# Performance work log

Measured on AMD Instinct MI355X. Metric: run time of the kernel, lower is better.

Reference implementation:

```python
import jax, jax.numpy as jnp
import numpy as np

DIM = 128
N_NODES = 50000
N_EDGES = 625000


def setup_inputs() -> dict:
    key = jax.random.key(0)
    ks = jax.random.split(key, 6)
    X = jax.random.normal(ks[0], (N_NODES, DIM), dtype=jnp.float32)
    edge_index = jax.random.randint(ks[1], (2, N_EDGES), 0, N_NODES, dtype=jnp.int64)
    # Linear params, init like torch (uniform +/- 1/sqrt(dim))
    bound = 1.0 / np.sqrt(DIM)
    msg_w = jax.random.uniform(ks[2], (DIM, DIM), minval=-bound, maxval=bound, dtype=jnp.float32)
    msg_b = jax.random.uniform(ks[3], (DIM,), minval=-bound, maxval=bound, dtype=jnp.float32)
    lin_w = jax.random.uniform(ks[4], (DIM, DIM), minval=-bound, maxval=bound, dtype=jnp.float32)
    lin_b = jax.random.uniform(ks[5], (DIM,), minval=-bound, maxval=bound, dtype=jnp.float32)
    eps = jnp.asarray(0.0, dtype=jnp.float32)
    return {"X": X, "edge_index": edge_index, "eps": eps,
            "msg_w": msg_w, "msg_b": msg_b, "lin_w": lin_w, "lin_b": lin_b}


def reference(X, edge_index, eps, msg_w, msg_b, lin_w, lin_b):
    src, dst = edge_index[0], edge_index[1]
    # msg_lin(X) then gather at dst: (E, F)
    msg = (jnp.einsum('nf,gf->ng', X, msg_w) + msg_b)[dst]
    # scatter-add messages onto src nodes: (N, F)
    agg = jax.ops.segment_sum(msg, src, num_segments=X.shape[0])
    out = (1.0 + eps) * X + agg
    out = jnp.einsum('nf,gf->ng', out, lin_w) + lin_b
    return jax.nn.relu(out)
```

## Files before the change

kernel.cpp:

```cpp
#include <hip/hip_runtime.h>
#include <hip/hip_bf16.h>

#define NN 50000
#define NE 625000
#define DIM 128

#define NBKT 782
#define NBKTP 784
#define CAP 1536
#define CHUNK 2048
#define NCHUNK ((NE + CHUNK - 1) / CHUNK)

#define XCAST_NB 6250
#define PREP_NB 65
#define BIN_B0 (XCAST_NB + PREP_NB)
#define SETUP_NB (BIN_B0 + NCHUNK)

using fragAB = __attribute__((ext_vector_type(8))) short;
using fragC  = __attribute__((ext_vector_type(4))) float;

__device__ __forceinline__ unsigned short f2bf(float f) {
    unsigned int u = __float_as_uint(f);
    unsigned int r = u + 0x7FFFu + ((u >> 16) & 1u);
    return (unsigned short)(r >> 16);
}

__device__ __forceinline__ float bflo(unsigned v) { return __uint_as_float(v << 16); }
__device__ __forceinline__ float bfhi(unsigned v) { return __uint_as_float(v & 0xffff0000u); }

__global__ __launch_bounds__(256) void setup_kernel(
    const float* __restrict__ X, const int* __restrict__ ei,
    const float* __restrict__ L, const float* __restrict__ W,
    const float* __restrict__ mb, float* __restrict__ cb,
    unsigned short* __restrict__ Bh, unsigned short* __restrict__ Xbf,
    int* __restrict__ bucket_cursor, unsigned* __restrict__ staging) {
    int blk = blockIdx.x;
    int t = threadIdx.x;

    if (blk < XCAST_NB) {
        int idx = (blk * 256 + t) * 4;
        float4 v = *(const float4*)(X + idx);
        uint2 p;
        p.x = (unsigned)f2bf(v.x) | ((unsigned)f2bf(v.y) << 16);
        p.y = (unsigned)f2bf(v.z) | ((unsigned)f2bf(v.w) << 16);
        *(uint2*)(Xbf + idx) = p;
        return;
    }
    if (blk < BIN_B0) {
        int idx = (blk - XCAST_NB) * 256 + t;
        if (idx < DIM * DIM) {
            int o = idx >> 7, g = idx & 127;
            float s = 0.f;
            for (int f = 0; f < DIM; f++) s += L[o * DIM + f] * W[f * DIM + g];
            Bh[o * 256 + 128 + g] = f2bf(s);
            Bh[o * 256 + g] = f2bf(L[o * DIM + g]);
        } else if (idx < DIM * DIM + DIM) {
            int o = idx - DIM * DIM;
            float s = 0.f;
            for (int f = 0; f < DIM; f++) s += L[o * DIM + f] * mb[f];
            cb[o] = s;
        }
        return;
    }

    __shared__ int cnt[NBKTP];
    __shared__ int base[NBKTP];
    __shared__ int gb[NBKTP];
    __shared__ int sarr[256];
    __shared__ unsigned staged[CHUNK];
    int e0 = (blk - BIN_B0) * CHUNK;
    int nthis = NE - e0; if (nthis > CHUNK) nthis = CHUNK;

    for (int i = t; i < NBKTP; i += 256) cnt[i] = 0;
    __syncthreads();

    unsigned pk[CHUNK / 256];
#pragma unroll
    for (int i = 0; i < CHUNK / 256; i++) {
        int e = e0 + i * 256 + t;
        if (e < NE) {
            int s = ei[e];
            int d = ei[NE + e];
            unsigned b = (unsigned)s >> 6;
            pk[i] = (b << 22) | ((unsigned)(s & 63) << 16) | (unsigned)d;
            atomicAdd(&cnt[b], 1);
        } else pk[i] = 0xFFFFFFFFu;
    }
    __syncthreads();

    int myb = t * 4;
    int s0 = 0;
    if (myb < NBKTP) s0 = cnt[myb] + cnt[myb + 1] + cnt[myb + 2] + cnt[myb + 3];
    sarr[t] = s0;
    __syncthreads();
    for (int off = 1; off < 256; off <<= 1) {
        int v = (t >= off) ? sarr[t - off] : 0;
        __syncthreads();
        sarr[t] += v;
        __syncthreads();
    }
    int run = sarr[t] - s0;
    if (myb < NBKTP) {
        for (int i = 0; i < 4; i++) {
            int b = myb + i;
            base[b] = run;
            int c = cnt[b];
            gb[b] = (b < NBKT && c > 0) ? atomicAdd(&bucket_cursor[b], c) : 0;
            run += c;
        }
    }
    __syncthreads();
    if (myb < NBKTP) {
        for (int i = 0; i < 4; i++) cnt[myb + i] = base[myb + i];
    }
    __syncthreads();

#pragma unroll
    for (int i = 0; i < CHUNK / 256; i++) {
        if (pk[i] != 0xFFFFFFFFu) {
            unsigned b = pk[i] >> 22;
            int pos = atomicAdd(&cnt[b], 1);
            staged[pos] = pk[i];
        }
    }
    __syncthreads();

    for (int idx = t; idx < nthis; idx += 256) {
        unsigned p = staged[idx];
        unsigned b = p >> 22;
        int pos = gb[b] + (idx - base[b]);
        if (pos < CAP) staging[(size_t)b * CAP + pos] = p;
    }
}

__global__ __launch_bounds__(256) void bucket_sort(const int* __restrict__ bucket_cursor,
                                                   const unsigned* __restrict__ staging,
                                                   int* __restrict__ deg, int* __restrict__ offs,
                                                   int* __restrict__ sdst) {
    __shared__ unsigned rec[CAP];
    __shared__ unsigned sorted_[CAP];
    __shared__ int hcnt[64];
    __shared__ int hbase[64];
    __shared__ int cur[64];
    int t = threadIdx.x;
    int b = blockIdx.x;
    int cnt_b = bucket_cursor[b];
    if (cnt_b > CAP) cnt_b = CAP;
    int base_b = b * CAP;

    if (t < 64) hcnt[t] = 0;
    __syncthreads();
    for (int i = t; i < cnt_b; i += 256) {
        unsigned r = staging[(size_t)b * CAP + i];
        rec[i] = r;
        atomicAdd(&hcnt[(r >> 16) & 63], 1);
    }
    __syncthreads();
    if (t == 0) {
        int run = 0;
        for (int i = 0; i < 64; i++) { hbase[i] = run; run += hcnt[i]; }
    }
    __syncthreads();
    if (t < 64) {
        cur[t] = hbase[t];
        int src = b * 64 + t;
        if (src < NN) {
            deg[src] = hcnt[t];
            offs[src] = base_b + hbase[t];
        }
    }
    __syncthreads();
    for (int i = t; i < cnt_b; i += 256) {
        unsigned r = rec[i];
        int pos = atomicAdd(&cur[(r >> 16) & 63], 1);
        sorted_[pos] = r;
    }
    __syncthreads();
    for (int i = t; i < cnt_b; i += 256)
        sdst[base_b + i] = (int)(sorted_[i] & 0xFFFFu);
}

__global__ __launch_bounds__(256) void gather_kernel(const int* __restrict__ offs,
                                                     const int* __restrict__ deg,
                                                     const int* __restrict__ sdst,
                                                     const unsigned short* __restrict__ Xbf,
                                                     unsigned short* __restrict__ Aggbf) {
    int wave = (blockIdx.x * 256 + threadIdx.x) >> 6;
    int lane = threadIdx.x & 63;
    if (wave >= NN) return;
    int start = __builtin_amdgcn_readfirstlane(offs[wave]);
    int cnt = __builtin_amdgcn_readfirstlane(deg[wave]);
    const unsigned* __restrict__ Xd = (const unsigned*)Xbf;
    float ax = 0.f, ay = 0.f;
    int j = 0;
    for (; j + 8 <= cnt; j += 8) {
        int d0 = sdst[start + j + 0];
        int d1 = sdst[start + j + 1];
        int d2 = sdst[start + j + 2];
        int d3 = sdst[start + j + 3];
        int d4 = sdst[start + j + 4];
        int d5 = sdst[start + j + 5];
        int d6 = sdst[start + j + 6];
        int d7 = sdst[start + j + 7];
        unsigned v0 = Xd[(size_t)d0 * 64 + lane];
        unsigned v1 = Xd[(size_t)d1 * 64 + lane];
        unsigned v2 = Xd[(size_t)d2 * 64 + lane];
        unsigned v3 = Xd[(size_t)d3 * 64 + lane];
        unsigned v4 = Xd[(size_t)d4 * 64 + lane];
        unsigned v5 = Xd[(size_t)d5 * 64 + lane];
        unsigned v6 = Xd[(size_t)d6 * 64 + lane];
        unsigned v7 = Xd[(size_t)d7 * 64 + lane];
        ax += bflo(v0) + bflo(v1) + bflo(v2) + bflo(v3) +
              bflo(v4) + bflo(v5) + bflo(v6) + bflo(v7);
        ay += bfhi(v0) + bfhi(v1) + bfhi(v2) + bfhi(v3) +
              bfhi(v4) + bfhi(v5) + bfhi(v6) + bfhi(v7);
    }
    if (j + 4 <= cnt) {
        int d0 = sdst[start + j + 0];
        int d1 = sdst[start + j + 1];
        int d2 = sdst[start + j + 2];
        int d3 = sdst[start + j + 3];
        unsigned v0 = Xd[(size_t)d0 * 64 + lane];
        unsigned v1 = Xd[(size_t)d1 * 64 + lane];
        unsigned v2 = Xd[(size_t)d2 * 64 + lane];
        unsigned v3 = Xd[(size_t)d3 * 64 + lane];
        ax += bflo(v0) + bflo(v1) + bflo(v2) + bflo(v3);
        ay += bfhi(v0) + bfhi(v1) + bfhi(v2) + bfhi(v3);
        j += 4;
    }
    for (; j < cnt; j++) {
        int d = sdst[start + j];
        unsigned v = Xd[(size_t)d * 64 + lane];
        ax += bflo(v);
        ay += bfhi(v);
    }
    unsigned packed = (unsigned)f2bf(ax) | ((unsigned)f2bf(ay) << 16);
    ((unsigned*)Aggbf)[(size_t)wave * 64 + lane] = packed;
}

__global__ __launch_bounds__(256) void outgemm_kernel(
    const unsigned short* __restrict__ Xbf, const unsigned short* __restrict__ Aggbf,
    const unsigned short* __restrict__ Bh, const int* __restrict__ deg,
    const float* __restrict__ cb, const float* __restrict__ lin_b,
    const float* __restrict__ epsp, float* __restrict__ out) {
    __shared__ unsigned short As[128 * 40];
    __shared__ unsigned short Bs[128 * 40];
    int tid = threadIdx.x;
    int lane = tid & 63;
    int wave = tid >> 6;
    int m16 = lane & 15;
    int quad = lane >> 4;
    int waveM = (wave & 1) * 64;
    int waveN = (wave >> 1) * 64;
    int r0 = blockIdx.x * 128;
    float scale = 1.0f + *epsp;

    fragC acc[4][4];
#pragma unroll
    for (int i = 0; i < 4; i++)
#pragma unroll
        for (int j = 0; j < 4; j++) acc[i][j] = (fragC){0.f, 0.f, 0.f, 0.f};

    int srow = tid >> 1;
    int shalf = tid & 1;
    int arow = r0 + srow;
    if (arow >= NN) arow = NN - 1;

    for (int kc = 0; kc < 8; kc++) {
        int kb = kc * 32;
        {
            const unsigned short* asrc = (kc < 4) ? Xbf : Aggbf;
            int akb = kb & 127;
            const uint4* gp = (const uint4*)(asrc + (size_t)arow * 128 + akb + shalf * 16);
            uint4 w0 = gp[0];
            uint4 w1 = gp[1];
            uint4* lp = (uint4*)(As + srow * 40 + shalf * 16);
            lp[0] = w0;
            lp[1] = w1;
        }
        {
            const uint4* gp = (const uint4*)(Bh + (size_t)srow * 256 + kb + shalf * 16);
            uint4 w0 = gp[0];
            uint4 w1 = gp[1];
            if (kb < 128) {
                unsigned int* u0 = (unsigned int*)&w0;
                unsigned int* u1 = (unsigned int*)&w1;
#pragma unroll
                for (int q = 0; q < 4; q++) {
                    float lo = bflo(u0[q]) * scale;
                    float hi = bfhi(u0[q]) * scale;
                    u0[q] = (unsigned)f2bf(lo) | ((unsigned)f2bf(hi) << 16);
                    lo = bflo(u1[q]) * scale;
                    hi = bfhi(u1[q]) * scale;
                    u1[q] = (unsigned)f2bf(lo) | ((unsigned)f2bf(hi) << 16);
                }
            }
            uint4* lp = (uint4*)(Bs + srow * 40 + shalf * 16);
            lp[0] = w0;
            lp[1] = w1;
        }
        __syncthreads();

        fragAB a[4], bfr[4];
#pragma unroll
        for (int i = 0; i < 4; i++)
            a[i] = *(const fragAB*)(As + (waveM + i * 16 + m16) * 40 + quad * 8);
#pragma unroll
        for (int j = 0; j < 4; j++)
            bfr[j] = *(const fragAB*)(Bs + (waveN + j * 16 + m16) * 40 + quad * 8);
#pragma unroll
        for (int i = 0; i < 4; i++)
#pragma unroll
            for (int j = 0; j < 4; j++)
                acc[i][j] = __builtin_amdgcn_mfma_f32_16x16x32_bf16(a[i], bfr[j], acc[i][j], 0, 0, 0);
        __syncthreads();
    }

#pragma unroll
    for (int j = 0; j < 4; j++) {
        int col = waveN + j * 16 + m16;
        float cbc = cb[col];
        float lbc = lin_b[col];
#pragma unroll
        for (int i = 0; i < 4; i++) {
            int rbase = r0 + waveM + i * 16 + quad * 4;
#pragma unroll
            for (int r = 0; r < 4; r++) {
                int row = rbase + r;
                if (row < NN) {
                    float dg = (float)deg[row];
                    float v = acc[i][j][r] + dg * cbc + lbc;
                    out[(size_t)row * 128 + col] = fmaxf(v, 0.f);
                }
            }
        }
    }
}

extern "C" void kernel_launch(void* const* d_in, const int* in_sizes, int n_in,
                              void* d_out, int out_size, void* d_ws, size_t ws_size,
                              hipStream_t stream) {
    const float* X = (const float*)d_in[0];
    const int* ei = (const int*)d_in[1];
    const float* epsp = (const float*)d_in[2];
    const float* msg_w = (const float*)d_in[3];
    const float* msg_b = (const float*)d_in[4];
    const float* lin_w = (const float*)d_in[5];
    const float* lin_b = (const float*)d_in[6];
    float* out = (float*)d_out;

    int* bucket_cursor = (int*)d_ws;
    unsigned* staging = (unsigned*)(bucket_cursor + 800);
    int* sdst = (int*)(staging + (size_t)NBKT * CAP);
    int* deg = sdst + (size_t)NBKT * CAP;
    int* offs = deg + NN;
    float* cb = (float*)(offs + NN);
    unsigned short* Bh = (unsigned short*)(cb + DIM);
    unsigned short* Xbf = Bh + 128 * 256;
    unsigned short* Aggbf = Xbf + (size_t)NN * 128;

    hipMemsetAsync(bucket_cursor, 0, NBKT * sizeof(int), stream);

    setup_kernel<<<SETUP_NB, 256, 0, stream>>>(X, ei, lin_w, msg_w, msg_b, cb, Bh, Xbf,
                                               bucket_cursor, staging);
    bucket_sort<<<NBKT, 256, 0, stream>>>(bucket_cursor, staging, deg, offs, sdst);
    gather_kernel<<<(NN * 64 + 255) / 256, 256, 0, stream>>>(offs, deg, sdst, Xbf, Aggbf);
    outgemm_kernel<<<(NN + 127) / 128, 256, 0, stream>>>(Xbf, Aggbf, Bh, deg, cb, lin_b,
                                                         epsp, out);
}
```

Before: 171.3 us.

## Split setup into prep and bin kernels, gather two edges per wave

The combined setup kernel is split into a cast/prep kernel and a separate binning kernel. The prep kernel now zeroes the bucket cursors itself, which removes the memset. The binning chunk size is halved, so more blocks are launched and each needs less shared memory, and a guard against negative positions is added. The gather kernel now has each half-wave load a different neighbor with 8-byte loads, then combines the halves with a cross-lane shuffle, putting more independent loads in flight per wave. The cost is one extra kernel launch and the shuffle reduction.

Measured after the change: 206.7 us. 1.21x slower.

```diff
diff --git a/kernel.cpp b/kernel.cpp
--- a/kernel.cpp
+++ b/kernel.cpp
@@ -8,13 +8,12 @@
 #define NBKT 782
 #define NBKTP 784
 #define CAP 1536
-#define CHUNK 2048
+#define CHUNK 1024
 #define NCHUNK ((NE + CHUNK - 1) / CHUNK)
 
 #define XCAST_NB 6250
 #define PREP_NB 65
-#define BIN_B0 (XCAST_NB + PREP_NB)
-#define SETUP_NB (BIN_B0 + NCHUNK)
+#define A_NB (XCAST_NB + PREP_NB + 1)
 
 using fragAB = __attribute__((ext_vector_type(8))) short;
 using fragC  = __attribute__((ext_vector_type(4))) float;
@@ -28,12 +27,11 @@
 __device__ __forceinline__ float bflo(unsigned v) { return __uint_as_float(v << 16); }
 __device__ __forceinline__ float bfhi(unsigned v) { return __uint_as_float(v & 0xffff0000u); }
 
-__global__ __launch_bounds__(256) void setup_kernel(
-    const float* __restrict__ X, const int* __restrict__ ei,
-    const float* __restrict__ L, const float* __restrict__ W,
-    const float* __restrict__ mb, float* __restrict__ cb,
-    unsigned short* __restrict__ Bh, unsigned short* __restrict__ Xbf,
-    int* __restrict__ bucket_cursor, unsigned* __restrict__ staging) {
+__global__ __launch_bounds__(256) void prep_cast_kernel(
+    const float* __restrict__ X, const float* __restrict__ L,
+    const float* __restrict__ W, const float* __restrict__ mb,
+    float* __restrict__ cb, unsigned short* __restrict__ Bh,
+    unsigned short* __restrict__ Xbf, int* __restrict__ bucket_cursor) {
     int blk = blockIdx.x;
     int t = threadIdx.x;
 
@@ -46,7 +44,7 @@
         *(uint2*)(Xbf + idx) = p;
         return;
     }
-    if (blk < BIN_B0) {
+    if (blk < XCAST_NB + PREP_NB) {
         int idx = (blk - XCAST_NB) * 256 + t;
         if (idx < DIM * DIM) {
             int o = idx >> 7, g = idx & 127;
@@ -62,13 +60,19 @@
         }
         return;
     }
-
+    for (int i = t; i < NBKTP; i += 256) bucket_cursor[i] = 0;
+}
+
+__global__ __launch_bounds__(256) void bin_kernel(const int* __restrict__ ei,
+                                                  int* __restrict__ bucket_cursor,
+                                                  unsigned* __restrict__ staging) {
     __shared__ int cnt[NBKTP];
     __shared__ int base[NBKTP];
     __shared__ int gb[NBKTP];
     __shared__ int sarr[256];
     __shared__ unsigned staged[CHUNK];
-    int e0 = (blk - BIN_B0) * CHUNK;
+    int t = threadIdx.x;
+    int e0 = blockIdx.x * CHUNK;
     int nthis = NE - e0; if (nthis > CHUNK) nthis = CHUNK;
 
     for (int i = t; i < NBKTP; i += 256) cnt[i] = 0;
@@ -129,7 +133,7 @@
         unsigned p = staged[idx];
         unsigned b = p >> 22;
         int pos = gb[b] + (idx - base[b]);
-        if (pos < CAP) staging[(size_t)b * CAP + pos] = p;
+        if (pos >= 0 && pos < CAP) staging[(size_t)b * CAP + pos] = p;
     }
 }
 
@@ -188,54 +192,56 @@
     int wave = (blockIdx.x * 256 + threadIdx.x) >> 6;
     int lane = threadIdx.x & 63;
     if (wave >= NN) return;
+    int l32 = lane & 31;
+    int half = lane >> 5;
     int start = __builtin_amdgcn_readfirstlane(offs[wave]);
     int cnt = __builtin_amdgcn_readfirstlane(deg[wave]);
-    const unsigned* __restrict__ Xd = (const unsigned*)Xbf;
-    float ax = 0.f, ay = 0.f;
+    const uint2* __restrict__ X2 = (const uint2*)Xbf;
+    float a0 = 0.f, a1 = 0.f, a2 = 0.f, a3 = 0.f;
+
+    int pairs = cnt >> 1;
     int j = 0;
-    for (; j + 8 <= cnt; j += 8) {
-        int d0 = sdst[start + j + 0];
-        int d1 = sdst[start + j + 1];
-        int d2 = sdst[start + j + 2];
-        int d3 = sdst[start + j + 3];
-        int d4 = sdst[start + j + 4];
-        int d5 = sdst[start + j + 5];
-        int d6 = sdst[start + j + 6];
-        int d7 = sdst[start + j + 7];
-        unsigned v0 = Xd[(size_t)d0 * 64 + lane];
-        unsigned v1 = Xd[(size_t)d1 * 64 + lane];
-        unsigned v2 = Xd[(size_t)d2 * 64 + lane];
-        unsigned v3 = Xd[(size_t)d3 * 64 + lane];
-        unsigned v4 = Xd[(size_t)d4 * 64 + lane];
-        unsigned v5 = Xd[(size_t)d5 * 64 + lane];
-        unsigned v6 = Xd[(size_t)d6 * 64 + lane];
-        unsigned v7 = Xd[(size_t)d7 * 64 + lane];
-        ax += bflo(v0) + bflo(v1) + bflo(v2) + bflo(v3) +
-              bflo(v4) + bflo(v5) + bflo(v6) + bflo(v7);
-        ay += bfhi(v0) + bfhi(v1) + bfhi(v2) + bfhi(v3) +
-              bfhi(v4) + bfhi(v5) + bfhi(v6) + bfhi(v7);
-    }
-    if (j + 4 <= cnt) {
-        int d0 = sdst[start + j + 0];
-        int d1 = sdst[start + j + 1];
-        int d2 = sdst[start + j + 2];
-        int d3 = sdst[start + j + 3];
-        unsigned v0 = Xd[(size_t)d0 * 64 + lane];
-        unsigned v1 = Xd[(size_t)d1 * 64 + lane];
-        unsigned v2 = Xd[(size_t)d2 * 64 + lane];
-        unsigned v3 = Xd[(size_t)d3 * 64 + lane];
-        ax += bflo(v0) + bflo(v1) + bflo(v2) + bflo(v3);
-        ay += bfhi(v0) + bfhi(v1) + bfhi(v2) + bfhi(v3);
-        j += 4;
-    }
-    for (; j < cnt; j++) {
-        int d = sdst[start + j];
-        unsigned v = Xd[(size_t)d * 64 + lane];
-        ax += bflo(v);
-        ay += bfhi(v);
-    }
-    unsigned packed = (unsigned)f2bf(ax) | ((unsigned)f2bf(ay) << 16);
-    ((unsigned*)Aggbf)[(size_t)wave * 64 + lane] = packed;
+    for (; j + 8 <= pairs; j += 8) {
+        int d[8];
+#pragma unroll
+        for (int i = 0; i < 8; i++) d[i] = sdst[start + 2 * (j + i) + half];
+        uint2 v[8];
+#pragma unroll
+        for (int i = 0; i < 8; i++) v[i] = X2[(size_t)d[i] * 32 + l32];
+#pragma unroll
+        for (int i = 0; i < 8; i++) {
+            a0 += bflo(v[i].x);
+            a1 += bfhi(v[i].x);
+            a2 += bflo(v[i].y);
+            a3 += bfhi(v[i].y);
+        }
+    }
+    for (; j < pairs; j++) {
+        int d = sdst[start + 2 * j + half];
+        uint2 v = X2[(size_t)d * 32 + l32];
+        a0 += bflo(v.x);
+        a1 += bfhi(v.x);
+        a2 += bflo(v.y);
+        a3 += bfhi(v.y);
+    }
+    if ((cnt & 1) && half == 0) {
+        int d = sdst[start + cnt - 1];
+        uint2 v = X2[(size_t)d * 32 + l32];
+        a0 += bflo(v.x);
+        a1 += bfhi(v.x);
+        a2 += bflo(v.y);
+        a3 += bfhi(v.y);
+    }
+    a0 += __shfl_xor(a0, 32);
+    a1 += __shfl_xor(a1, 32);
+    a2 += __shfl_xor(a2, 32);
+    a3 += __shfl_xor(a3, 32);
+    if (half == 0) {
+        uint2 p;
+        p.x = (unsigned)f2bf(a0) | ((unsigned)f2bf(a1) << 16);
+        p.y = (unsigned)f2bf(a2) | ((unsigned)f2bf(a3) << 16);
+        ((uint2*)Aggbf)[(size_t)wave * 32 + l32] = p;
+    }
 }
 
 __global__ __launch_bounds__(256) void outgemm_kernel(
@@ -359,10 +365,9 @@
     unsigned short* Xbf = Bh + 128 * 256;
     unsigned short* Aggbf = Xbf + (size_t)NN * 128;
 
-    hipMemsetAsync(bucket_cursor, 0, NBKT * sizeof(int), stream);
-
-    setup_kernel<<<SETUP_NB, 256, 0, stream>>>(X, ei, lin_w, msg_w, msg_b, cb, Bh, Xbf,
-                                               bucket_cursor, staging);
+    prep_cast_kernel<<<A_NB, 256, 0, stream>>>(X, lin_w, msg_w, msg_b, cb, Bh, Xbf,
+                                               bucket_cursor);
+    bin_kernel<<<NCHUNK, 256, 0, stream>>>(ei, bucket_cursor, staging);
     bucket_sort<<<NBKT, 256, 0, stream>>>(bucket_cursor, staging, deg, offs, sdst);
     gather_kernel<<<(NN * 64 + 255) / 256, 256, 0, stream>>>(offs, deg, sdst, Xbf, Aggbf);
     outgemm_kernel<<<(NN + 127) / 128, 256, 0, stream>>>(Xbf, Aggbf, Bh, deg, cb, lin_b,
```
